# Performance work log

Hardware: AMD Instinct MI355X
Metric: run time of the kernel (lower is better)

Reference implementation:

```python
import jax, jax.numpy as jnp
import numpy as np

FEAT_DIM = 256
NUM_HEADS = 8
HEAD_DIM = FEAT_DIM // NUM_HEADS
N_NODES = 4096
LN_EPS = 1e-5


def setup_inputs() -> dict:
    key = jax.random.key(0)
    ks = jax.random.split(key, 10)
    C = FEAT_DIM
    s = 1.0 / np.sqrt(C)
    x = jax.random.normal(ks[0], (N_NODES, C), dtype=jnp.float32)
    Wq = jax.random.uniform(ks[1], (C, C), jnp.float32, -s, s)
    bq = jax.random.uniform(ks[2], (C,), jnp.float32, -s, s)
    Wk = jax.random.uniform(ks[3], (C, C), jnp.float32, -s, s)
    bk = jax.random.uniform(ks[4], (C,), jnp.float32, -s, s)
    Wv = jax.random.uniform(ks[5], (C, C), jnp.float32, -s, s)
    bv = jax.random.uniform(ks[6], (C,), jnp.float32, -s, s)
    Wo = jax.random.uniform(ks[7], (C, C), jnp.float32, -s, s)
    bo = jax.random.uniform(ks[8], (C,), jnp.float32, -s, s)
    scale = jnp.float32(1.0 / np.sqrt(HEAD_DIM))
    gamma = jnp.ones((C,), jnp.float32)
    beta = jnp.zeros((C,), jnp.float32)
    return {"x": x, "Wq": Wq, "bq": bq, "Wk": Wk, "bk": bk, "Wv": Wv,
            "bv": bv, "scale": scale, "Wo": Wo, "bo": bo,
            "gamma": gamma, "beta": beta}


def reference(x, Wq, bq, Wk, bk, Wv, bv, scale, Wo, bo, gamma, beta):
    N, C = x.shape
    H, D = NUM_HEADS, HEAD_DIM
    q = (x @ Wq + bq).reshape(N, H, D)
    k = (x @ Wk + bk).reshape(N, H, D)
    v = (x @ Wv + bv).reshape(N, H, D)
    # scores[i, j, h]; softmax over j (the key/node axis), per original dim=1
    scores = jnp.einsum('ihd,jhd->ijh', q, k) * scale
    attn = jax.nn.softmax(scores, axis=1)
    messages = jnp.einsum('ijh,jhd->ihd', attn, v).reshape(N, H * D)
    y = x + messages @ Wo + bo
    # LayerNorm over last dim
    mu = jnp.mean(y, axis=-1, keepdims=True)
    var = jnp.mean(jnp.square(y - mu), axis=-1, keepdims=True)
    return (y - mu) * jax.lax.rsqrt(var + LN_EPS) * gamma + beta
```

## Files before the change

### kernel.cpp

```cpp
#include <hip/hip_runtime.h>
#include <hip/hip_bf16.h>
#include <math.h>

#define NN 4096
#define C  256
#define NH 8
#define HD 32
#define LN_EPS 1e-5f
#define LOG2E 1.44269504088896340736f

#define NZ 4
#define ZT (NN / NZ)
#define TQB 128
#define NIT (ZT / 64)

typedef unsigned short u16;
typedef __attribute__((ext_vector_type(8))) short bf16x8;
typedef __attribute__((ext_vector_type(4))) float f32x4;
typedef __attribute__((ext_vector_type(16))) float f32x16;

__device__ inline u16 f2b(float f) {
    union { float f; unsigned u; } v; v.f = f;
    unsigned r = (v.u + 0x7fff + ((v.u >> 16) & 1)) >> 16;
    return (u16)r;
}

__device__ inline float fexp2(float x) {
#if __has_builtin(__builtin_amdgcn_exp2f)
    return __builtin_amdgcn_exp2f(x);
#else
    return exp2f(x);
#endif
}

__device__ inline unsigned pack_trunc(float e0, float e1) {
    return __builtin_amdgcn_perm(__float_as_uint(e1), __float_as_uint(e0),
                                 0x07060302u);
}

__device__ inline f32x16 zero16() {
    return f32x16{0.f,0.f,0.f,0.f, 0.f,0.f,0.f,0.f,
                  0.f,0.f,0.f,0.f, 0.f,0.f,0.f,0.f};
}

template<int c>
__device__ inline bf16x8 softmax_chunk(const f32x16 s, float& lsum) {
    const float e0 = fexp2(s[8*c+0]);
    const float e1 = fexp2(s[8*c+1]);
    const float e2 = fexp2(s[8*c+2]);
    const float e3 = fexp2(s[8*c+3]);
    const float e4 = fexp2(s[8*c+4]);
    const float e5 = fexp2(s[8*c+5]);
    const float e6 = fexp2(s[8*c+6]);
    const float e7 = fexp2(s[8*c+7]);
    lsum += ((e0 + e1) + (e2 + e3)) + ((e4 + e5) + (e6 + e7));
    const unsigned p01 = pack_trunc(e0, e1);
    const unsigned p23 = pack_trunc(e2, e3);
    const unsigned p45 = pack_trunc(e4, e5);
    const unsigned p67 = pack_trunc(e6, e7);
    const auto w02 = __builtin_amdgcn_permlane32_swap(p01, p45, false, false);
    const auto w13 = __builtin_amdgcn_permlane32_swap(p23, p67, false, false);
    union { unsigned w[4]; bf16x8 v; } pa;
    pa.w[0] = w02[0]; pa.w[1] = w13[0];
    pa.w[2] = w02[1]; pa.w[3] = w13[1];
    return pa.v;
}

__global__ __launch_bounds__(256) void prep_kernel(
    const float* __restrict__ Wq, const float* __restrict__ Wk,
    const float* __restrict__ Wv, const float* __restrict__ Wo,
    u16* __restrict__ WqkvT, u16* __restrict__ WoT)
{
    __shared__ float tile[32][33];
    const int z = blockIdx.z;
    const float* W = (z == 0) ? Wq : (z == 1) ? Wk : (z == 2) ? Wv : Wo;
    u16* WT = (z == 3) ? WoT : (WqkvT + (size_t)z * 256 * 256);
    const int tx = threadIdx.x & 31, ty = threadIdx.x >> 5;
    const int n0 = blockIdx.x * 32, k0 = blockIdx.y * 32;
    #pragma unroll
    for (int i = 0; i < 32; i += 8)
        tile[ty + i][tx] = W[(size_t)(k0 + ty + i) * 256 + n0 + tx];
    __syncthreads();
    #pragma unroll
    for (int i = 0; i < 32; i += 8)
        WT[(size_t)(n0 + ty + i) * 256 + k0 + tx] = f2b(tile[tx][ty + i]);
}

__global__ __launch_bounds__(256) void qkv_mfma_kernel(
    const float* __restrict__ x, const u16* __restrict__ WT,
    const float* __restrict__ bq, const float* __restrict__ bk,
    const float* __restrict__ bv, const float* __restrict__ scale_p,
    u16* __restrict__ qb, u16* __restrict__ kb, u16* __restrict__ vT)
{
    const int m0 = blockIdx.x * 64;
    const int n0 = blockIdx.y * 64;
    const int t = threadIdx.x;
    const int wave = t >> 6, lane = t & 63;
    const int l16 = lane & 15, quad = lane >> 4;

    f32x4 acc[4];
    #pragma unroll
    for (int ct = 0; ct < 4; ++ct) acc[ct] = f32x4{0.f, 0.f, 0.f, 0.f};

    const float* xrow = x + (size_t)(m0 + wave * 16 + l16) * C;
    #pragma unroll
    for (int kk = 0; kk < 8; ++kk) {
        const float4 a0 = *(const float4*)(xrow + kk * 32 + quad * 8);
        const float4 a1 = *(const float4*)(xrow + kk * 32 + quad * 8 + 4);
        union { __hip_bfloat162 h2[4]; bf16x8 v; } af;
        af.h2[0] = __float22bfloat162_rn(float2{a0.x, a0.y});
        af.h2[1] = __float22bfloat162_rn(float2{a0.z, a0.w});
        af.h2[2] = __float22bfloat162_rn(float2{a1.x, a1.y});
        af.h2[3] = __float22bfloat162_rn(float2{a1.z, a1.w});
        #pragma unroll
        for (int ct = 0; ct < 4; ++ct) {
            const bf16x8 bfr = *(const bf16x8*)(
                WT + (size_t)(n0 + ct * 16 + l16) * C + kk * 32 + quad * 8);
            acc[ct] = __builtin_amdgcn_mfma_f32_16x16x32_bf16(af.v, bfr, acc[ct], 0, 0, 0);
        }
    }

    const int sect = n0 >> 8;
    const int c0 = n0 & 255;
    const int rbase = m0 + wave * 16 + quad * 4;
    if (sect == 0) {
        const float scl = (*scale_p) * LOG2E;
        #pragma unroll
        for (int ct = 0; ct < 4; ++ct) {
            const int c = c0 + ct * 16 + l16;
            const float b = bq[c];
            #pragma unroll
            for (int r = 0; r < 4; ++r)
                qb[(size_t)(rbase + r) * C + c] = f2b((acc[ct][r] + b) * scl);
        }
    } else if (sect == 1) {
        #pragma unroll
        for (int ct = 0; ct < 4; ++ct) {
            const int c = c0 + ct * 16 + l16;
            const float b = bk[c];
            #pragma unroll
            for (int r = 0; r < 4; ++r)
                kb[(size_t)(rbase + r) * C + c] = f2b(acc[ct][r] + b);
        }
    } else {
        #pragma unroll
        for (int ct = 0; ct < 4; ++ct) {
            const int c = c0 + ct * 16 + l16;
            const float b = bv[c];
            union { u16 u[4]; unsigned long long ull; } pk;
            #pragma unroll
            for (int r = 0; r < 4; ++r) pk.u[r] = f2b(acc[ct][r] + b);
            *(unsigned long long*)(vT + (size_t)c * NN + rbase) = pk.ull;
        }
    }
}

__global__ __launch_bounds__(256) void attn_mfma_kernel(
    const u16* __restrict__ q, const u16* __restrict__ k,
    const u16* __restrict__ vT, float* __restrict__ msgp,
    float* __restrict__ lp)
{
    __shared__ u16 Ks[2][2048];
    __shared__ u16 Vs[2][2048];

    const int h = blockIdx.y, z = blockIdx.z;
    const int t = threadIdx.x;
    const int w = t >> 6, lane = t & 63;
    const int l31 = lane & 31, hi = lane >> 5;
    const int qbase = blockIdx.x * TQB + w * 32;

    const u16* qrp = q + (size_t)(qbase + l31) * C + h * HD + hi * 8;
    const bf16x8 qf0 = *(const bf16x8*)(qrp);
    const bf16x8 qf1 = *(const bf16x8*)(qrp + 16);

    f32x16 o = zero16();
    float lsum = 0.f;

    const int sst = w >> 1, sfc = w & 1;
    const u16* gk = k + (size_t)(z * ZT + sst * 32 + l31) * C
                      + h * HD + sfc * 16 + hi * 8;
    const u16* gv = vT + (size_t)(h * HD + l31) * NN
                       + z * ZT + sst * 32 + sfc * 16 + hi * 8;

    bf16x8 kreg = *(const bf16x8*)(gk);
    bf16x8 vreg = *(const bf16x8*)(gv);

    for (int it = 0; it < NIT; ++it) {
        const int b = it & 1;
        *(bf16x8*)(&Ks[b][w * 512 + lane * 8]) = kreg;
        *(bf16x8*)(&Vs[b][w * 512 + lane * 8]) = vreg;
        __syncthreads();

        if (it + 1 < NIT) {
            kreg = *(const bf16x8*)(gk + (size_t)(it + 1) * 64 * C);
            vreg = *(const bf16x8*)(gv + (it + 1) * 64);
        }

        const u16* KsB = Ks[b];
        const u16* VsB = Vs[b];
        #pragma unroll
        for (int s = 0; s < 2; ++s) {
            const bf16x8 kf0 = *(const bf16x8*)(KsB + (s * 2 + 0) * 512 + lane * 8);
            const bf16x8 kf1 = *(const bf16x8*)(KsB + (s * 2 + 1) * 512 + lane * 8);
            const bf16x8 vf0 = *(const bf16x8*)(VsB + (s * 2 + 0) * 512 + lane * 8);
            const bf16x8 vf1 = *(const bf16x8*)(VsB + (s * 2 + 1) * 512 + lane * 8);

            f32x16 sA = zero16();
            sA = __builtin_amdgcn_mfma_f32_32x32x16_bf16(kf0, qf0, sA, 0, 0, 0);
            sA = __builtin_amdgcn_mfma_f32_32x32x16_bf16(kf1, qf1, sA, 0, 0, 0);
            const bf16x8 pa0 = softmax_chunk<0>(sA, lsum);
            o = __builtin_amdgcn_mfma_f32_32x32x16_bf16(pa0, vf0, o, 0, 0, 0);
            const bf16x8 pa1 = softmax_chunk<1>(sA, lsum);
            o = __builtin_amdgcn_mfma_f32_32x32x16_bf16(pa1, vf1, o, 0, 0, 0);
        }
        __syncthreads();
    }

    lsum += __shfl_xor(lsum, 32);
    if (hi == 0)
        lp[((size_t)z * NH + h) * NN + qbase + l31] = lsum;

    #pragma unroll
    for (int r = 0; r < 16; ++r) {
        const int qr = qbase + (r & 3) + 8 * (r >> 2) + 4 * hi;
        msgp[((size_t)z * NN + qr) * C + h * HD + l31] = o[r];
    }
}

#define OROWS 8
__global__ __launch_bounds__(256) void out_ln_mfma_kernel(
    const float* __restrict__ msgp, const float* __restrict__ lp,
    const u16* __restrict__ WoT, const float* __restrict__ bo,
    const float* __restrict__ x, const float* __restrict__ gamma,
    const float* __restrict__ beta, float* __restrict__ out)
{
    __shared__ float sums[2][4][OROWS];
    const int m0 = blockIdx.x * OROWS;
    const int t = threadIdx.x;
    const int w = t >> 6, lane = t & 63;
    const int l16 = lane & 15, quad = lane >> 4;

    f32x4 acc[4];
    #pragma unroll
    for (int ct = 0; ct < 4; ++ct) acc[ct] = f32x4{0.f, 0.f, 0.f, 0.f};

    const int ar = min(m0 + l16, NN - 1);
    #pragma unroll
    for (int kk = 0; kk < 8; ++kk) {
        float l = 0.f;
        #pragma unroll
        for (int z = 0; z < NZ; ++z)
            l += lp[((size_t)z * NH + kk) * NN + ar];
        const float li = 1.f / l;

        float4 a0 = float4{0.f, 0.f, 0.f, 0.f};
        float4 a1 = float4{0.f, 0.f, 0.f, 0.f};
        #pragma unroll
        for (int z = 0; z < NZ; ++z) {
            const float* arow = msgp + ((size_t)z * NN + ar) * C;
            const float4 b0 = *(const float4*)(arow + kk * 32 + quad * 8);
            const float4 b1 = *(const float4*)(arow + kk * 32 + quad * 8 + 4);
            a0.x += b0.x; a0.y += b0.y; a0.z += b0.z; a0.w += b0.w;
            a1.x += b1.x; a1.y += b1.y; a1.z += b1.z; a1.w += b1.w;
        }

        union { __hip_bfloat162 h2[4]; bf16x8 v; } af;
        af.h2[0] = __float22bfloat162_rn(float2{a0.x * li, a0.y * li});
        af.h2[1] = __float22bfloat162_rn(float2{a0.z * li, a0.w * li});
        af.h2[2] = __float22bfloat162_rn(float2{a1.x * li, a1.y * li});
        af.h2[3] = __float22bfloat162_rn(float2{a1.z * li, a1.w * li});
        #pragma unroll
        for (int ct = 0; ct < 4; ++ct) {
            const bf16x8 bfr = *(const bf16x8*)(
                WoT + (size_t)(w * 64 + ct * 16 + l16) * C + kk * 32 + quad * 8);
            acc[ct] = __builtin_amdgcn_mfma_f32_16x16x32_bf16(af.v, bfr, acc[ct], 0, 0, 0);
        }
    }

    float val[4][4];
    if (quad < 2) {
        #pragma unroll
        for (int r = 0; r < 4; ++r) {
            const int row = m0 + quad * 4 + r;
            float sr = 0.f, qr = 0.f;
            #pragma unroll
            for (int ct = 0; ct < 4; ++ct) {
                const int c = w * 64 + ct * 16 + l16;
                const float v = acc[ct][r] + bo[c] + x[(size_t)row * C + c];
                val[ct][r] = v;
                sr += v;
                qr = fmaf(v, v, qr);
            }
            sr += __shfl_xor(sr, 1); sr += __shfl_xor(sr, 2);
            sr += __shfl_xor(sr, 4); sr += __shfl_xor(sr, 8);
            qr += __shfl_xor(qr, 1); qr += __shfl_xor(qr, 2);
            qr += __shfl_xor(qr, 4); qr += __shfl_xor(qr, 8);
            if (l16 == 0) {
                sums[0][w][quad * 4 + r] = sr;
                sums[1][w][quad * 4 + r] = qr;
            }
        }
    }
    __syncthreads();

    if (quad < 2) {
        #pragma unroll
        for (int r = 0; r < 4; ++r) {
            const int ri = quad * 4 + r;
            const int row = m0 + ri;
            const float tot  = sums[0][0][ri] + sums[0][1][ri] + sums[0][2][ri] + sums[0][3][ri];
            const float tot2 = sums[1][0][ri] + sums[1][1][ri] + sums[1][2][ri] + sums[1][3][ri];
            const float mu = tot * (1.f / C);
            const float var = fmaxf(tot2 * (1.f / C) - mu * mu, 0.f);
            const float rstd = rsqrtf(var + LN_EPS);
            #pragma unroll
            for (int ct = 0; ct < 4; ++ct) {
                const int c = w * 64 + ct * 16 + l16;
                out[(size_t)row * C + c] = (val[ct][r] - mu) * rstd * gamma[c] + beta[c];
            }
        }
    }
}

extern "C" void kernel_launch(void* const* d_in, const int* in_sizes, int n_in,
                              void* d_out, int out_size, void* d_ws, size_t ws_size,
                              hipStream_t stream) {
    const float* x     = (const float*)d_in[0];
    const float* Wq    = (const float*)d_in[1];
    const float* bq    = (const float*)d_in[2];
    const float* Wk    = (const float*)d_in[3];
    const float* bk    = (const float*)d_in[4];
    const float* Wv    = (const float*)d_in[5];
    const float* bv    = (const float*)d_in[6];
    const float* scale = (const float*)d_in[7];
    const float* Wo    = (const float*)d_in[8];
    const float* bo    = (const float*)d_in[9];
    const float* gamma = (const float*)d_in[10];
    const float* beta  = (const float*)d_in[11];
    float* out = (float*)d_out;

    u16* qb     = (u16*)d_ws;
    u16* kb     = qb + (size_t)NN * C;
    u16* vT     = kb + (size_t)NN * C;
    u16* WqkvT  = vT + (size_t)NN * C;
    u16* WoT    = WqkvT + (size_t)3 * C * C;
    float* msgp = (float*)(WoT + (size_t)C * C);
    float* lp   = msgp + (size_t)NZ * NN * C;

    prep_kernel<<<dim3(8, 8, 4), 256, 0, stream>>>(Wq, Wk, Wv, Wo,
                                                   WqkvT, WoT);
    qkv_mfma_kernel<<<dim3(NN / 64, 12), 256, 0, stream>>>(
        x, WqkvT, bq, bk, bv, scale, qb, kb, vT);
    attn_mfma_kernel<<<dim3(NN / TQB, NH, NZ), 256, 0, stream>>>(
        qb, kb, vT, msgp, lp);
    out_ln_mfma_kernel<<<NN / OROWS, 256, 0, stream>>>(msgp, lp, WoT, bo, x,
                                                       gamma, beta, out);
}
```

Before: 154.0 us.

## Process two query tiles per wave, double key splits, widen output-LN row tile

Each attention wave now handles 64 queries (two 32-row MFMA tiles) that share each K/V fragment loaded from shared memory, which halves LDS traffic per query. The key axis is split into 8 partitions instead of 4 so the grid keeps enough blocks. The output projection and LayerNorm kernel now processes 16 rows per block, so all MFMA lanes do useful work, and the clamp and quad guards are removed. The trade-off is more register pressure from two accumulators and twice as many partial message buffers written to and read back from global memory.

Measured after the change: 152.8 us. Within noise of the previous version (-0.8%).

```diff
diff --git a/kernel.cpp b/kernel.cpp
--- a/kernel.cpp
+++ b/kernel.cpp
@@ -9,9 +9,9 @@
 #define LN_EPS 1e-5f
 #define LOG2E 1.44269504088896340736f
 
-#define NZ 4
+#define NZ 8
 #define ZT (NN / NZ)
-#define TQB 128
+#define TQB 256
 #define NIT (ZT / 64)
 
 typedef unsigned short u16;
@@ -167,14 +167,17 @@
     const int t = threadIdx.x;
     const int w = t >> 6, lane = t & 63;
     const int l31 = lane & 31, hi = lane >> 5;
-    const int qbase = blockIdx.x * TQB + w * 32;
-
-    const u16* qrp = q + (size_t)(qbase + l31) * C + h * HD + hi * 8;
-    const bf16x8 qf0 = *(const bf16x8*)(qrp);
-    const bf16x8 qf1 = *(const bf16x8*)(qrp + 16);
-
-    f32x16 o = zero16();
-    float lsum = 0.f;
+    const int qbase = blockIdx.x * TQB + w * 64;
+
+    const u16* qrpA = q + (size_t)(qbase + l31) * C + h * HD + hi * 8;
+    const bf16x8 qf0a = *(const bf16x8*)(qrpA);
+    const bf16x8 qf1a = *(const bf16x8*)(qrpA + 16);
+    const u16* qrpB = qrpA + 32 * C;
+    const bf16x8 qf0b = *(const bf16x8*)(qrpB);
+    const bf16x8 qf1b = *(const bf16x8*)(qrpB + 16);
+
+    f32x16 oA = zero16(), oB = zero16();
+    float lsA = 0.f, lsB = 0.f;
 
     const int sst = w >> 1, sfc = w & 1;
     const u16* gk = k + (size_t)(z * ZT + sst * 32 + l31) * C
@@ -206,28 +209,40 @@
             const bf16x8 vf1 = *(const bf16x8*)(VsB + (s * 2 + 1) * 512 + lane * 8);
 
             f32x16 sA = zero16();
-            sA = __builtin_amdgcn_mfma_f32_32x32x16_bf16(kf0, qf0, sA, 0, 0, 0);
-            sA = __builtin_amdgcn_mfma_f32_32x32x16_bf16(kf1, qf1, sA, 0, 0, 0);
-            const bf16x8 pa0 = softmax_chunk<0>(sA, lsum);
-            o = __builtin_amdgcn_mfma_f32_32x32x16_bf16(pa0, vf0, o, 0, 0, 0);
-            const bf16x8 pa1 = softmax_chunk<1>(sA, lsum);
-            o = __builtin_amdgcn_mfma_f32_32x32x16_bf16(pa1, vf1, o, 0, 0, 0);
+            sA = __builtin_amdgcn_mfma_f32_32x32x16_bf16(kf0, qf0a, sA, 0, 0, 0);
+            sA = __builtin_amdgcn_mfma_f32_32x32x16_bf16(kf1, qf1a, sA, 0, 0, 0);
+            const bf16x8 paA0 = softmax_chunk<0>(sA, lsA);
+            oA = __builtin_amdgcn_mfma_f32_32x32x16_bf16(paA0, vf0, oA, 0, 0, 0);
+            const bf16x8 paA1 = softmax_chunk<1>(sA, lsA);
+            oA = __builtin_amdgcn_mfma_f32_32x32x16_bf16(paA1, vf1, oA, 0, 0, 0);
+
+            f32x16 sB = zero16();
+            sB = __builtin_amdgcn_mfma_f32_32x32x16_bf16(kf0, qf0b, sB, 0, 0, 0);
+            sB = __builtin_amdgcn_mfma_f32_32x32x16_bf16(kf1, qf1b, sB, 0, 0, 0);
+            const bf16x8 paB0 = softmax_chunk<0>(sB, lsB);
+            oB = __builtin_amdgcn_mfma_f32_32x32x16_bf16(paB0, vf0, oB, 0, 0, 0);
+            const bf16x8 paB1 = softmax_chunk<1>(sB, lsB);
+            oB = __builtin_amdgcn_mfma_f32_32x32x16_bf16(paB1, vf1, oB, 0, 0, 0);
         }
         __syncthreads();
     }
 
-    lsum += __shfl_xor(lsum, 32);
-    if (hi == 0)
-        lp[((size_t)z * NH + h) * NN + qbase + l31] = lsum;
+    lsA += __shfl_xor(lsA, 32);
+    lsB += __shfl_xor(lsB, 32);
+    if (hi == 0) {
+        lp[((size_t)z * NH + h) * NN + qbase + l31] = lsA;
+        lp[((size_t)z * NH + h) * NN + qbase + 32 + l31] = lsB;
+    }
 
     #pragma unroll
     for (int r = 0; r < 16; ++r) {
-        const int qr = qbase + (r & 3) + 8 * (r >> 2) + 4 * hi;
-        msgp[((size_t)z * NN + qr) * C + h * HD + l31] = o[r];
-    }
-}
-
-#define OROWS 8
+        const int qrA = qbase + (r & 3) + 8 * (r >> 2) + 4 * hi;
+        msgp[((size_t)z * NN + qrA) * C + h * HD + l31] = oA[r];
+        msgp[((size_t)z * NN + qrA + 32) * C + h * HD + l31] = oB[r];
+    }
+}
+
+#define OROWS 16
 __global__ __launch_bounds__(256) void out_ln_mfma_kernel(
     const float* __restrict__ msgp, const float* __restrict__ lp,
     const u16* __restrict__ WoT, const float* __restrict__ bo,
@@ -244,7 +259,7 @@
     #pragma unroll
     for (int ct = 0; ct < 4; ++ct) acc[ct] = f32x4{0.f, 0.f, 0.f, 0.f};
 
-    const int ar = min(m0 + l16, NN - 1);
+    const int ar = m0 + l16;
     #pragma unroll
     for (int kk = 0; kk < 8; ++kk) {
         float l = 0.f;
@@ -278,46 +293,42 @@
     }
 
     float val[4][4];
-    if (quad < 2) {
-        #pragma unroll
-        for (int r = 0; r < 4; ++r) {
-            const int row = m0 + quad * 4 + r;
-            float sr = 0.f, qr = 0.f;
-            #pragma unroll
-            for (int ct = 0; ct < 4; ++ct) {
-                const int c = w * 64 + ct * 16 + l16;
-                const float v = acc[ct][r] + bo[c] + x[(size_t)row * C + c];
-                val[ct][r] = v;
-                sr += v;
-                qr = fmaf(v, v, qr);
-            }
-            sr += __shfl_xor(sr, 1); sr += __shfl_xor(sr, 2);
-            sr += __shfl_xor(sr, 4); sr += __shfl_xor(sr, 8);
-            qr += __shfl_xor(qr, 1); qr += __shfl_xor(qr, 2);
-            qr += __shfl_xor(qr, 4); qr += __shfl_xor(qr, 8);
-            if (l16 == 0) {
-                sums[0][w][quad * 4 + r] = sr;
-                sums[1][w][quad * 4 + r] = qr;
-            }
+    #pragma unroll
+    for (int r = 0; r < 4; ++r) {
+        const int row = m0 + quad * 4 + r;
+        float sr = 0.f, qr = 0.f;
+        #pragma unroll
+        for (int ct = 0; ct < 4; ++ct) {
+            const int c = w * 64 + ct * 16 + l16;
+            const float v = acc[ct][r] + bo[c] + x[(size_t)row * C + c];
+            val[ct][r] = v;
+            sr += v;
+            qr = fmaf(v, v, qr);
+        }
+        sr += __shfl_xor(sr, 1); sr += __shfl_xor(sr, 2);
+        sr += __shfl_xor(sr, 4); sr += __shfl_xor(sr, 8);
+        qr += __shfl_xor(qr, 1); qr += __shfl_xor(qr, 2);
+        qr += __shfl_xor(qr, 4); qr += __shfl_xor(qr, 8);
+        if (l16 == 0) {
+            sums[0][w][quad * 4 + r] = sr;
+            sums[1][w][quad * 4 + r] = qr;
         }
     }
     __syncthreads();
 
-    if (quad < 2) {
-        #pragma unroll
-        for (int r = 0; r < 4; ++r) {
-            const int ri = quad * 4 + r;
-            const int row = m0 + ri;
-            const float tot  = sums[0][0][ri] + sums[0][1][ri] + sums[0][2][ri] + sums[0][3][ri];
-            const float tot2 = sums[1][0][ri] + sums[1][1][ri] + sums[1][2][ri] + sums[1][3][ri];
-            const float mu = tot * (1.f / C);
-            const float var = fmaxf(tot2 * (1.f / C) - mu * mu, 0.f);
-            const float rstd = rsqrtf(var + LN_EPS);
-            #pragma unroll
-            for (int ct = 0; ct < 4; ++ct) {
-                const int c = w * 64 + ct * 16 + l16;
-                out[(size_t)row * C + c] = (val[ct][r] - mu) * rstd * gamma[c] + beta[c];
-            }
+    #pragma unroll
+    for (int r = 0; r < 4; ++r) {
+        const int ri = quad * 4 + r;
+        const int row = m0 + ri;
+        const float tot  = sums[0][0][ri] + sums[0][1][ri] + sums[0][2][ri] + sums[0][3][ri];
+        const float tot2 = sums[1][0][ri] + sums[1][1][ri] + sums[1][2][ri] + sums[1][3][ri];
+        const float mu = tot * (1.f / C);
+        const float var = fmaxf(tot2 * (1.f / C) - mu * mu, 0.f);
+        const float rstd = rsqrtf(var + LN_EPS);
+        #pragma unroll
+        for (int ct = 0; ct < 4; ++ct) {
+            const int c = w * 64 + ct * 16 + l16;
+            out[(size_t)row * C + c] = (val[ct][r] - mu) * rstd * gamma[c] + beta[c];
         }
     }
 }
```
